# Optimization experiments

Measured on AMD Instinct MI355X. Metric: run time of the kernel, lower is better.

Reference implementation:

```python
import jax, jax.numpy as jnp
import numpy as np

K = 9
DILATION = 2


def pairwise_distance(x):
    # x: (B, N, C) -> (B, N, N) squared Euclidean distances
    x_inner = -2.0 * jnp.einsum('bnc,bmc->bnm', x, x)
    x_square = jnp.sum(x * x, axis=-1, keepdims=True)  # (B, N, 1)
    return x_square + x_inner + jnp.swapaxes(x_square, 1, 2)


def setup_inputs() -> dict:
    key = jax.random.key(0)
    x = jax.random.normal(key, (4, 64, 4096, 1), dtype=jnp.float32)
    return {"x": x}


def reference(x):
    # x: (B, C, N, 1) -> (B, N, C)
    xt = jnp.swapaxes(x, 1, 2)[..., 0]
    B, N, C = xt.shape
    k_eff = K * DILATION
    neg_dist = -pairwise_distance(xt)  # (B, N, N)
    _, nn_idx = jax.lax.top_k(neg_dist, k_eff)  # (B, N, k_eff)
    center_idx = jnp.broadcast_to(jnp.arange(N)[None, :, None], (B, N, k_eff))
    edge_index = jnp.stack((nn_idx, center_idx), axis=0)  # (2, B, N, k_eff)
    # dilated selection: every DILATION-th neighbor -> (2, B, N, K)
    return edge_index[:, :, :, ::DILATION]
```

## Files before the change

kernel.cpp:

```cpp
#include <hip/hip_runtime.h>


#pragma clang fp contract(off)

#define BB    4
#define CDIM  64
#define NPTS  4096
#define KSEL  17
#define KOUT  9
#define QB    2

__global__ __launch_bounds__(256) void knn_sq(const float* __restrict__ x,
                                              float* __restrict__ sq) {
#pragma clang fp contract(off)
    int g = blockIdx.x * 256 + threadIdx.x;
    int b = g >> 12;
    int m = g & (NPTS - 1);
    const float* xb = x + (size_t)b * CDIM * NPTS + m;

    float a[CDIM];
    #pragma unroll
    for (int c = 0; c < CDIM; ++c) {
        float v = xb[c * NPTS];
        a[c] = v * v;
    }
    float s16[16];
    #pragma unroll
    for (int i = 0; i < 16; ++i)
        s16[i] = (a[i] + a[i + 16]) + (a[i + 32] + a[i + 48]);
    float t8[8];
    #pragma unroll
    for (int i = 0; i < 8; ++i) t8[i] = s16[i] + s16[i + 8];
    float t4[4];
    #pragma unroll
    for (int i = 0; i < 4; ++i) t4[i] = t8[i] + t8[i + 4];
    float u0 = t4[0] + t4[2];
    float u1 = t4[1] + t4[3];
    sq[g] = u0 + u1;
}

#define DO_QUERY(ACC, QI)                                                      \
    {                                                                          \
        const float sqn = sqb[n0 + (QI)];                                      \
        _Pragma("unroll")                                                      \
        for (int j = 0; j < 16; ++j) {                                         \
            float inner = -2.0f * ACC[j];                   \
            float t1    = sqn + inner;                                         \
            ACC[j]      = t1 + sqm[j];            \
        }                                                                      \
        unsigned mask = 0;                                                     \
        float cm = 3.0e38f;                                                    \
        int   ci = 0x7fffffff;                                                 \
        _Pragma("unroll")                                                      \
        for (int j = 0; j < 16; ++j) {                                         \
            float v = ACC[j];                                                  \
            if (v < cm) { cm = v; ci = 16 * t + j; }                           \
        }                                                                      \
        int myOut = 0;                                                         \
        for (int r = 0; r < KSEL; ++r) {                                       \
            const int p = ((QI) + r) & 1;              \
            float bd = cm;                                                     \
            int   bi = ci;                                                     \
            _Pragma("unroll")                                                  \
            for (int off = 32; off >= 1; off >>= 1) {                          \
                float od = __shfl_down(bd, off);                               \
                int   oi = __shfl_down(bi, off);                               \
                if (od < bd || (od == bd && oi < bi)) { bd = od; bi = oi; }    \
            }                                                                  \
            if ((t & 63) == 0) { redD[p][t >> 6] = bd; redI[p][t >> 6] = bi; } \
            __syncthreads();                                                   \
            float gb = redD[p][0];                                             \
            int   gi = redI[p][0];                                             \
            _Pragma("unroll")                                                  \
            for (int w = 1; w < 4; ++w) {                                      \
                float od = redD[p][w];                                         \
                int   oi = redI[p][w];                                         \
                if (od < gb || (od == gb && oi < gi)) { gb = od; gi = oi; }    \
            }                                                                  \
            if (t < KOUT && r == 2 * t) myOut = gi;    \
            if ((gi >> 4) == t) {                      \
                mask |= 1u << (gi & 15);                                       \
                cm = 3.0e38f; ci = 0x7fffffff;                                 \
                _Pragma("unroll")                                              \
                for (int j = 0; j < 16; ++j) {                                 \
                    float v = ACC[j];                                          \
                    if (!((mask >> j) & 1u) && v < cm) { cm = v; ci = 16 * t + j; } \
                }                                                              \
            }                                                                  \
        }                                                                      \
        if (t < KOUT) {                                                        \
            int    nq   = n0 + (QI);                                           \
            size_t base = (size_t)((b << 12) + nq) * KOUT;                     \
            out[base + t] = myOut;                                             \
            out[(size_t)BB * NPTS * KOUT + base + t] = nq;                     \
        }                                                                      \
    }

__global__ __launch_bounds__(256, 4) void knn_main(const float* __restrict__ x,
                                                   const float* __restrict__ sq,
                                                   int* __restrict__ out) {
#pragma clang fp contract(off)
    const int blk = blockIdx.x;
    const int b   = blk >> 11;
    const int n0  = (blk & 2047) * QB;
    const int t   = threadIdx.x;

    __shared__ float qs[QB][CDIM];
    __shared__ float redD[2][4];
    __shared__ int   redI[2][4];

    const float* xb = x + (size_t)b * CDIM * NPTS;

    if (t < QB * CDIM) {
        int q = t >> 6, c = t & 63;
        qs[q][c] = xb[c * NPTS + n0 + q];
    }
    __syncthreads();

    const float* sqb = sq + (b << 12);

    float acc0[16], acc1[16];
    {
        const float4* xr = (const float4*)(xb + 16 * t);
        float4 v0 = xr[0], v1 = xr[1], v2 = xr[2], v3 = xr[3];
        float xv[16] = {v0.x, v0.y, v0.z, v0.w, v1.x, v1.y, v1.z, v1.w,
                        v2.x, v2.y, v2.z, v2.w, v3.x, v3.y, v3.z, v3.w};
        float q0 = qs[0][0], q1 = qs[1][0];
        #pragma unroll
        for (int j = 0; j < 16; ++j) {
            acc0[j] = q0 * xv[j];
            acc1[j] = q1 * xv[j];
        }
    }
    #pragma unroll 2
    for (int c = 1; c < CDIM; ++c) {
        const float4* xr = (const float4*)(xb + c * NPTS + 16 * t);
        float4 v0 = xr[0], v1 = xr[1], v2 = xr[2], v3 = xr[3];
        float xv[16] = {v0.x, v0.y, v0.z, v0.w, v1.x, v1.y, v1.z, v1.w,
                        v2.x, v2.y, v2.z, v2.w, v3.x, v3.y, v3.z, v3.w};
        float q0 = qs[0][c], q1 = qs[1][c];
        #pragma unroll
        for (int j = 0; j < 16; ++j) {
            float p0 = q0 * xv[j];
            acc0[j] = acc0[j] + p0;
            float p1 = q1 * xv[j];
            acc1[j] = acc1[j] + p1;
        }
    }

    float sqm[16];
    {
        const float4* sr = (const float4*)(sqb + 16 * t);
        float4 s0 = sr[0], s1 = sr[1], s2 = sr[2], s3 = sr[3];
        sqm[0]=s0.x; sqm[1]=s0.y; sqm[2]=s0.z; sqm[3]=s0.w;
        sqm[4]=s1.x; sqm[5]=s1.y; sqm[6]=s1.z; sqm[7]=s1.w;
        sqm[8]=s2.x; sqm[9]=s2.y; sqm[10]=s2.z; sqm[11]=s2.w;
        sqm[12]=s3.x; sqm[13]=s3.y; sqm[14]=s3.z; sqm[15]=s3.w;
    }

    DO_QUERY(acc0, 0)
    DO_QUERY(acc1, 1)
}

extern "C" void kernel_launch(void* const* d_in, const int* in_sizes, int n_in,
                              void* d_out, int out_size, void* d_ws, size_t ws_size,
                              hipStream_t stream) {
    const float* x   = (const float*)d_in[0];
    float*       sqv = (float*)d_ws;
    int*         out = (int*)d_out;

    hipLaunchKernelGGL(knn_sq,   dim3((BB * NPTS) / 256), dim3(256), 0, stream, x, sqv);
    hipLaunchKernelGGL(knn_main, dim3((BB * NPTS) / QB),  dim3(256), 0, stream, x, sqv, out);
}
```

Measured before the change: 543.0 us.

## Double-buffer dot-product loads and reduce only the winning wave per selection round

The channel loop now software-pipelines global loads with two register buffers and reads query values straight from global memory, which removes the shared-memory staging and its initial barrier. The top-k selection caches each wave's best candidate in shared memory, so each round only the wave that owned the last winner reruns its shuffle reduction. The other waves simply rewrite their cached value. This aims to cut shuffle work and latency in the 17 serial selection rounds, at the cost of more registers from the double buffers.

New measurement: 544.8 us. About the same (+0.3%).

```diff
diff --git a/kernel.cpp b/kernel.cpp
--- a/kernel.cpp
+++ b/kernel.cpp
@@ -38,63 +38,6 @@
     float u1 = t4[1] + t4[3];
     sq[g] = u0 + u1;
 }
-
-#define DO_QUERY(ACC, QI)                                                      \
-    {                                                                          \
-        const float sqn = sqb[n0 + (QI)];                                      \
-        _Pragma("unroll")                                                      \
-        for (int j = 0; j < 16; ++j) {                                         \
-            float inner = -2.0f * ACC[j];                   \
-            float t1    = sqn + inner;                                         \
-            ACC[j]      = t1 + sqm[j];            \
-        }                                                                      \
-        unsigned mask = 0;                                                     \
-        float cm = 3.0e38f;                                                    \
-        int   ci = 0x7fffffff;                                                 \
-        _Pragma("unroll")                                                      \
-        for (int j = 0; j < 16; ++j) {                                         \
-            float v = ACC[j];                                                  \
-            if (v < cm) { cm = v; ci = 16 * t + j; }                           \
-        }                                                                      \
-        int myOut = 0;                                                         \
-        for (int r = 0; r < KSEL; ++r) {                                       \
-            const int p = ((QI) + r) & 1;              \
-            float bd = cm;                                                     \
-            int   bi = ci;                                                     \
-            _Pragma("unroll")                                                  \
-            for (int off = 32; off >= 1; off >>= 1) {                          \
-                float od = __shfl_down(bd, off);                               \
-                int   oi = __shfl_down(bi, off);                               \
-                if (od < bd || (od == bd && oi < bi)) { bd = od; bi = oi; }    \
-            }                                                                  \
-            if ((t & 63) == 0) { redD[p][t >> 6] = bd; redI[p][t >> 6] = bi; } \
-            __syncthreads();                                                   \
-            float gb = redD[p][0];                                             \
-            int   gi = redI[p][0];                                             \
-            _Pragma("unroll")                                                  \
-            for (int w = 1; w < 4; ++w) {                                      \
-                float od = redD[p][w];                                         \
-                int   oi = redI[p][w];                                         \
-                if (od < gb || (od == gb && oi < gi)) { gb = od; gi = oi; }    \
-            }                                                                  \
-            if (t < KOUT && r == 2 * t) myOut = gi;    \
-            if ((gi >> 4) == t) {                      \
-                mask |= 1u << (gi & 15);                                       \
-                cm = 3.0e38f; ci = 0x7fffffff;                                 \
-                _Pragma("unroll")                                              \
-                for (int j = 0; j < 16; ++j) {                                 \
-                    float v = ACC[j];                                          \
-                    if (!((mask >> j) & 1u) && v < cm) { cm = v; ci = 16 * t + j; } \
-                }                                                              \
-            }                                                                  \
-        }                                                                      \
-        if (t < KOUT) {                                                        \
-            int    nq   = n0 + (QI);                                           \
-            size_t base = (size_t)((b << 12) + nq) * KOUT;                     \
-            out[base + t] = myOut;                                             \
-            out[(size_t)BB * NPTS * KOUT + base + t] = nq;                     \
-        }                                                                      \
-    }
 
 __global__ __launch_bounds__(256, 4) void knn_main(const float* __restrict__ x,
                                                    const float* __restrict__ sq,
@@ -105,48 +48,63 @@
     const int n0  = (blk & 2047) * QB;
     const int t   = threadIdx.x;
 
-    __shared__ float qs[QB][CDIM];
-    __shared__ float redD[2][4];
-    __shared__ int   redI[2][4];
-
-    const float* xb = x + (size_t)b * CDIM * NPTS;
-
-    if (t < QB * CDIM) {
-        int q = t >> 6, c = t & 63;
-        qs[q][c] = xb[c * NPTS + n0 + q];
-    }
-    __syncthreads();
-
+    __shared__ float wbK[QB][2][4];
+    __shared__ int   wbI[QB][2][4];
+
+    const float* xb  = x + (size_t)b * CDIM * NPTS;
+    const float* xq0 = xb + n0;
+    const float* xq1 = xb + n0 + 1;
     const float* sqb = sq + (b << 12);
+    const float* xp  = xb + 16 * t;
 
     float acc0[16], acc1[16];
+    float4 a0, a1, a2, a3, b0, b1, b2, b3;
+
+#define LOAD_A(CC) { const float4* _p = (const float4*)(xp + (size_t)(CC) * NPTS); \
+                     a0 = _p[0]; a1 = _p[1]; a2 = _p[2]; a3 = _p[3]; }
+#define LOAD_B(CC) { const float4* _p = (const float4*)(xp + (size_t)(CC) * NPTS); \
+                     b0 = _p[0]; b1 = _p[1]; b2 = _p[2]; b3 = _p[3]; }
+
+#define ACCUM(V0, V1, V2, V3, Q0, Q1)                                          \
+    { const float _xv[16] = {V0.x,V0.y,V0.z,V0.w, V1.x,V1.y,V1.z,V1.w,         \
+                             V2.x,V2.y,V2.z,V2.w, V3.x,V3.y,V3.z,V3.w};        \
+      _Pragma("unroll")                                                        \
+      for (int _j = 0; _j < 16; ++_j) {                                        \
+          float _p0 = (Q0) * _xv[_j];                             \
+          acc0[_j] = acc0[_j] + _p0;                   \
+          float _p1 = (Q1) * _xv[_j];                                          \
+          acc1[_j] = acc1[_j] + _p1;                                           \
+      } }
+
+    float qA0 = xq0[0],      qA1 = xq1[0];
+    float qB0 = xq0[NPTS],   qB1 = xq1[NPTS];
+    LOAD_A(0);
+    LOAD_B(1);
     {
-        const float4* xr = (const float4*)(xb + 16 * t);
-        float4 v0 = xr[0], v1 = xr[1], v2 = xr[2], v3 = xr[3];
-        float xv[16] = {v0.x, v0.y, v0.z, v0.w, v1.x, v1.y, v1.z, v1.w,
-                        v2.x, v2.y, v2.z, v2.w, v3.x, v3.y, v3.z, v3.w};
-        float q0 = qs[0][0], q1 = qs[1][0];
+        const float _xv[16] = {a0.x,a0.y,a0.z,a0.w, a1.x,a1.y,a1.z,a1.w,
+                               a2.x,a2.y,a2.z,a2.w, a3.x,a3.y,a3.z,a3.w};
         #pragma unroll
-        for (int j = 0; j < 16; ++j) {
-            acc0[j] = q0 * xv[j];
-            acc1[j] = q1 * xv[j];
+        for (int _j = 0; _j < 16; ++_j) {
+            acc0[_j] = qA0 * _xv[_j];
+            acc1[_j] = qA1 * _xv[_j];
         }
     }
-    #pragma unroll 2
-    for (int c = 1; c < CDIM; ++c) {
-        const float4* xr = (const float4*)(xb + c * NPTS + 16 * t);
-        float4 v0 = xr[0], v1 = xr[1], v2 = xr[2], v3 = xr[3];
-        float xv[16] = {v0.x, v0.y, v0.z, v0.w, v1.x, v1.y, v1.z, v1.w,
-                        v2.x, v2.y, v2.z, v2.w, v3.x, v3.y, v3.z, v3.w};
-        float q0 = qs[0][c], q1 = qs[1][c];
-        #pragma unroll
-        for (int j = 0; j < 16; ++j) {
-            float p0 = q0 * xv[j];
-            acc0[j] = acc0[j] + p0;
-            float p1 = q1 * xv[j];
-            acc1[j] = acc1[j] + p1;
-        }
-    }
+    qA0 = xq0[2 * NPTS]; qA1 = xq1[2 * NPTS];
+    LOAD_A(2);
+    ACCUM(b0, b1, b2, b3, qB0, qB1)
+    qB0 = xq0[3 * NPTS]; qB1 = xq1[3 * NPTS];
+
+    for (int c = 2; c <= 60; c += 2) {
+        LOAD_B(c + 1);
+        ACCUM(a0, a1, a2, a3, qA0, qA1)
+        qA0 = xq0[(size_t)(c + 2) * NPTS]; qA1 = xq1[(size_t)(c + 2) * NPTS];
+        LOAD_A(c + 2);
+        ACCUM(b0, b1, b2, b3, qB0, qB1)
+        qB0 = xq0[(size_t)(c + 3) * NPTS]; qB1 = xq1[(size_t)(c + 3) * NPTS];
+    }
+    LOAD_B(63);
+    ACCUM(a0, a1, a2, a3, qA0, qA1)
+    ACCUM(b0, b1, b2, b3, qB0, qB1)
 
     float sqm[16];
     {
@@ -158,8 +116,76 @@
         sqm[12]=s3.x; sqm[13]=s3.y; sqm[14]=s3.z; sqm[15]=s3.w;
     }
 
-    DO_QUERY(acc0, 0)
-    DO_QUERY(acc1, 1)
+#define WAVE_ARGMIN(BD, BI)                                                    \
+    _Pragma("unroll")                                                          \
+    for (int _off = 32; _off >= 1; _off >>= 1) {                               \
+        float _od = __shfl_down(BD, _off);                                     \
+        int   _oi = __shfl_down(BI, _off);                                     \
+        if (_od < BD || (_od == BD && _oi < BI)) { BD = _od; BI = _oi; }       \
+    }
+
+#define SELECT(ACC, QI)                                                        \
+    {                                                                          \
+        const float sqn = sqb[n0 + (QI)];                                      \
+        _Pragma("unroll")                                                      \
+        for (int j = 0; j < 16; ++j) {                                         \
+            float inner = -2.0f * ACC[j];                   \
+            float t1    = sqn + inner;                                         \
+            ACC[j]      = t1 + sqm[j];            \
+        }                                                                      \
+        unsigned mask = 0;                                                     \
+        float cm = 3.0e38f;                                                    \
+        int   ci = 0x7fffffff;                                                 \
+        _Pragma("unroll")                                                      \
+        for (int j = 0; j < 16; ++j) {                                         \
+            float v = ACC[j];                                                  \
+            if (v < cm) { cm = v; ci = 16 * t + j; }                           \
+        }                                                                      \
+        float bd = cm;                                                         \
+        int   bi = ci;                                                         \
+        WAVE_ARGMIN(bd, bi)                                                    \
+        if ((t & 63) == 0) { wbK[QI][0][t >> 6] = bd; wbI[QI][0][t >> 6] = bi; } \
+        __syncthreads();                                                       \
+        int myOut = 0;                                                         \
+        for (int r = 0; r < KSEL; ++r) {                                       \
+            const int p = r & 1;                                               \
+            float gb = wbK[QI][p][0];                                          \
+            int   gi = wbI[QI][p][0];                                          \
+            _Pragma("unroll")                                                  \
+            for (int w = 1; w < 4; ++w) {                                      \
+                float od = wbK[QI][p][w];                                      \
+                int   oi = wbI[QI][p][w];                                      \
+                if (od < gb || (od == gb && oi < gi)) { gb = od; gi = oi; }    \
+            }                                                                  \
+            if (t < KOUT && r == 2 * t) myOut = gi;    \
+            if (r + 1 < KSEL) {                                                \
+                if ((gi >> 10) == (t >> 6)) {            \
+                    if ((gi >> 4) == t) {              \
+                        mask |= 1u << (gi & 15);                               \
+                        cm = 3.0e38f; ci = 0x7fffffff;                         \
+                        _Pragma("unroll")                                      \
+                        for (int j = 0; j < 16; ++j) {                         \
+                            float v = ACC[j];                                  \
+                            if (!((mask >> j) & 1u) && v < cm) { cm = v; ci = 16 * t + j; } \
+                        }                                                      \
+                    }                                                          \
+                    bd = cm; bi = ci;                                          \
+                    WAVE_ARGMIN(bd, bi)                                        \
+                }                                                              \
+                if ((t & 63) == 0) { wbK[QI][p ^ 1][t >> 6] = bd; wbI[QI][p ^ 1][t >> 6] = bi; } \
+                __syncthreads();                                               \
+            }                                                                  \
+        }                                                                      \
+        if (t < KOUT) {                                                        \
+            int    nq   = n0 + (QI);                                           \
+            size_t base = (size_t)((b << 12) + nq) * KOUT;                     \
+            out[base + t] = myOut;                                             \
+            out[(size_t)BB * NPTS * KOUT + base + t] = nq;                     \
+        }                                                                      \
+    }
+
+    SELECT(acc0, 0)
+    SELECT(acc1, 1)
 }
 
 extern "C" void kernel_launch(void* const* d_in, const int* in_sizes, int n_in,
```
